# Performance work log

Hardware: AMD Instinct MI355X
Metric: run time of the kernel (lower is better)

The kernel has to match this reference:

```python
import jax, jax.numpy as jnp
import numpy as np
from jax import lax

B, C, W = 16, 64, 125000  # batch, EEG channels, raw samples
KH, KW, SW, OC = 3, 2500, 1250, 32


def setup_inputs() -> dict:
    key = jax.random.key(0)
    ks = jax.random.split(key, 10)
    inp = {
        "x": jax.random.normal(ks[0], (B, 1, C, W), dtype=jnp.float32),
        # Conv2d(1->32, kernel=(3,2500))
        "conv_w": jax.random.normal(ks[1], (OC, 1, KH, KW), dtype=jnp.float32) * 0.02,
        "conv_b": jax.random.normal(ks[2], (OC,), dtype=jnp.float32) * 0.02,
        # Conv2d(32->1, kernel=(1,1))
        "conv2_w": jax.random.normal(ks[3], (1, OC, 1, 1), dtype=jnp.float32) * 0.1,
        "conv2_b": jax.random.normal(ks[4], (1,), dtype=jnp.float32) * 0.1,
        # nn.RNN(input_size=1, hidden_size=1): scalar weights
        "w_ih": jax.random.normal(ks[5], (1, 1), dtype=jnp.float32),
        "w_hh": jax.random.normal(ks[6], (1, 1), dtype=jnp.float32),
        "b_ih": jax.random.normal(ks[7], (1,), dtype=jnp.float32) * 0.1,
        "b_hh": jax.random.normal(ks[8], (1,), dtype=jnp.float32) * 0.1,
        # torch.rand(num_layers=1, B, 1) hidden init, reused for every row i
        "h0": jax.random.uniform(ks[9], (1, B, 1), dtype=jnp.float32),
    }
    return inp


def reference(x, conv_w, conv_b, conv2_w, conv2_b, w_ih, w_hh, b_ih, b_hh, h0):
    # F.pad(x, (0,0,1,1), 'replicate'): pad channel (height) dim by 1 each side
    xp = jnp.pad(x, ((0, 0), (0, 0), (1, 1), (0, 0)), mode="edge")
    # conv + relu -> [B, 32, C, T]
    y = lax.conv_general_dilated(
        xp, conv_w, window_strides=(1, SW), padding="VALID",
        dimension_numbers=("NCHW", "OIHW", "NCHW"))
    y = jax.nn.relu(y + conv_b[None, :, None, None])
    # 1x1 conv 32->1 + relu -> [B, C, T]
    z = jnp.einsum("bohw,o->bhw", y, conv2_w[0, :, 0, 0]) + conv2_b[0]
    z = jax.nn.relu(z)
    # Elman RNN with scalar weights, scanned over T; carry is [B, C]
    wih, whh = w_ih[0, 0], w_hh[0, 0]
    bias = b_ih[0] + b_hh[0]
    h_init = jnp.broadcast_to(h0[0, :, 0][:, None], z.shape[:2])  # [B, C]

    def step(h, xt):  # xt: [B, C]
        h = jnp.tanh(wih * xt + whh * h + bias)
        return h, None

    xs = jnp.moveaxis(z, -1, 0)  # [T, B, C]
    h_final, _ = lax.scan(step, h_init, xs)
    return jax.nn.sigmoid(h_final)  # [B, C]
```

## Files before the change

kernel.cpp:

```cpp
#include <hip/hip_runtime.h>
#include <math.h>

#define B_ 16
#define C_ 64
#define J_ 100
#define T_ 99
#define KW_ 1250
#define KP_ 1280
#define N_ 192
#define M_ (B_*C_*J_)
#define BM 128
#define BK 32
#define NCHUNK 40

typedef __attribute__((ext_vector_type(8))) _Float16 half8;
typedef __attribute__((ext_vector_type(4))) float f32x4;
typedef __attribute__((ext_vector_type(2), aligned(8))) float f32x2;

#define GLD_LDS16(gp, lp) \
    __builtin_amdgcn_global_load_lds((const __attribute__((address_space(1))) void*)(gp), \
                                     (__attribute__((address_space(3))) void*)(lp), 16, 0, 0)

__global__ __launch_bounds__(256) void wconv_kernel(const float* __restrict__ cw,
                                                    _Float16* __restrict__ wh)
{
    int n = blockIdx.x;
    int o = n / 6, rem = n - o * 6, kh = rem >> 1, hf = rem & 1;
    const float* src = cw + o * 7500 + kh * 2500 + hf * 1250;
    for (int k = threadIdx.x; k < KP_; k += 256)
        wh[n * KP_ + k] = (k < KW_) ? (_Float16)src[k] : (_Float16)0.f;
}

__global__ __launch_bounds__(256, 2) void gemm_kernel(const float* __restrict__ x,
                                                      const _Float16* __restrict__ wh,
                                                      _Float16* __restrict__ P)
{
    __shared__ __align__(16) _Float16 smA[2][BM * BK];
    __shared__ __align__(16) _Float16 smB[3][N_ * BK];

    const int tid  = threadIdx.x;
    const int bm0  = blockIdx.x * BM;
    const int lane = tid & 63;
    const int wave = tid >> 6;
    const int wm   = (wave & 1) * 64;
    const int wn   = (wave >> 1) * 96;
    const int l15  = lane & 15;
    const int lq   = lane >> 4;

    const float* ap[2]; int koff[2]; int adst[2];
#pragma unroll
    for (int u = 0; u < 2; u++) {
        int q  = u * 256 + tid;
        int rl = q >> 2, p = q & 3;
        int gr = bm0 + rl;
        int b  = gr / 6400;
        int j  = (gr - b * 6400) >> 6;
        int c  = gr & 63;
        long xrow = (long)(b * 64 + c) * 100 + j;
        ap[u]   = x + xrow * KW_ + p * 8;
        koff[u] = p * 8;
        adst[u] = q * 8;
    }
    const _Float16* bp[3]; int bdst[3];
#pragma unroll
    for (int i = 0; i < 3; i++) {
        int qb = (i * 4 + wave) * 64 + lane;
        int n = qb >> 2, p = qb & 3;
        bp[i]   = wh + n * KP_ + p * 8;
        bdst[i] = (i * 4 + wave) * 512;
    }

    f32x4 acc[4][6];
#pragma unroll
    for (int mi = 0; mi < 4; mi++)
#pragma unroll
        for (int ni = 0; ni < 6; ni++) acc[mi][ni] = (f32x4){0.f, 0.f, 0.f, 0.f};

    f32x2 areg[2][2][4];
#define LOADA(k0, slot)                                                        \
    do {                                                                       \
        _Pragma("unroll") for (int u = 0; u < 2; u++)                          \
        _Pragma("unroll") for (int j2 = 0; j2 < 4; j2++) {                     \
            int k = (k0) + koff[u] + j2 * 2;           \
            areg[slot][u][j2] = (k + 2 <= KW_)                                 \
                ? *(const f32x2*)(ap[u] + (k0) + j2 * 2)                       \
                : (f32x2){0.f, 0.f};                                           \
        }                                                                      \
    } while (0)

#pragma unroll
    for (int i = 0; i < 3; i++) GLD_LDS16(bp[i], &smB[0][0] + bdst[i]);
#pragma unroll
    for (int i = 0; i < 3; i++) GLD_LDS16(bp[i] + BK, &smB[1][0] + bdst[i]);
    LOADA(0, 0);
    LOADA(BK, 1);

    int bi = 0;
    for (int ck = 0; ck < NCHUNK; ck++) {
        const int slot = ck & 1;
        _Float16* Ab = &smA[slot][0];
        _Float16* Bb = &smB[bi][0];

#pragma unroll
        for (int u = 0; u < 2; u++) {
            half8 h;
#pragma unroll
            for (int j2 = 0; j2 < 4; j2++) {
                h[2 * j2]     = (_Float16)areg[slot][u][j2].x;
                h[2 * j2 + 1] = (_Float16)areg[slot][u][j2].y;
            }
            *(half8*)(Ab + adst[u]) = h;
        }

        asm volatile("s_waitcnt lgkmcnt(0)" ::: "memory");
        if (ck == 0 || ck >= NCHUNK - 2) {
            asm volatile("s_waitcnt vmcnt(0)" ::: "memory");
        } else {
            asm volatile("s_waitcnt vmcnt(11)" ::: "memory");
        }
        __builtin_amdgcn_s_barrier();
        __builtin_amdgcn_sched_barrier(0);

        int bi2 = bi + 2; if (bi2 >= 3) bi2 -= 3;
        if (ck + 2 < NCHUNK) {
            _Float16* Bn = &smB[bi2][0];
            const int k2 = (ck + 2) * BK;
#pragma unroll
            for (int i = 0; i < 3; i++) GLD_LDS16(bp[i] + k2, Bn + bdst[i]);
        }
        if (ck + 2 < NCHUNK) LOADA((ck + 2) * BK, slot);

        half8 afr[4], bfr[6];
#pragma unroll
        for (int mi = 0; mi < 4; mi++)
            afr[mi] = *(const half8*)(Ab + (wm + mi * 16 + l15) * BK + lq * 8);
#pragma unroll
        for (int ni = 0; ni < 6; ni++)
            bfr[ni] = *(const half8*)(Bb + (wn + ni * 16 + l15) * BK + lq * 8);
#pragma unroll
        for (int mi = 0; mi < 4; mi++)
#pragma unroll
            for (int ni = 0; ni < 6; ni++)
                acc[mi][ni] = __builtin_amdgcn_mfma_f32_16x16x32_f16(
                    afr[mi], bfr[ni], acc[mi][ni], 0, 0, 0);

        bi = (bi == 2) ? 0 : bi + 1;
    }

#pragma unroll
    for (int mi = 0; mi < 4; mi++) {
        int mrow = bm0 + wm + mi * 16 + lq * 4;
#pragma unroll
        for (int ni = 0; ni < 6; ni++) {
            int n = wn + ni * 16 + l15;
#pragma unroll
            for (int r2 = 0; r2 < 4; r2++)
                P[(size_t)(mrow + r2) * N_ + n] = (_Float16)acc[mi][ni][r2];
        }
    }
#undef LOADA
}

__global__ __launch_bounds__(256) void combine_kernel(const _Float16* __restrict__ P,
                                                      const float* __restrict__ conv_b,
                                                      const float* __restrict__ c2w,
                                                      const float* __restrict__ c2b,
                                                      float* __restrict__ z)
{
    __shared__ float Pl[64][193];
    __shared__ float red[4][64];
    const int t   = blockIdx.x;
    const int b   = blockIdx.y;
    const int tid = threadIdx.x;
    const int c   = tid & 63;
    const int og  = tid >> 6;

    float v[8];
#pragma unroll
    for (int o = 0; o < 8; o++) v[o] = conv_b[og * 8 + o];

    for (int hf = 0; hf < 2; hf++) {
        const int j = t + hf;
        const _Float16* Pb = P + (size_t)((b * 100 + j) * 64) * N_;
        __syncthreads();
#pragma unroll
        for (int i = 0; i < 6; i++) {
            int e   = i * 256 + tid;
            half8 h = *(const half8*)(Pb + e * 8);
            int row = e / 24;
            int col = (e - row * 24) * 8;
#pragma unroll
            for (int u = 0; u < 8; u++) Pl[row][col + u] = (float)h[u];
        }
        __syncthreads();
#pragma unroll
        for (int kh = 0; kh < 3; kh++) {
            int r = c + kh - 1;
            r = r < 0 ? 0 : (r > 63 ? 63 : r);
#pragma unroll
            for (int o = 0; o < 8; o++)
                v[o] += Pl[r][(og * 8 + o) * 6 + kh * 2 + hf];
        }
    }

    float part = 0.f;
#pragma unroll
    for (int o = 0; o < 8; o++) part += fmaxf(v[o], 0.f) * c2w[og * 8 + o];
    red[og][c] = part;
    __syncthreads();
    if (og == 0) {
        float zz = red[0][c] + red[1][c] + red[2][c] + red[3][c] + c2b[0];
        z[t * (B_ * C_) + b * 64 + c] = fmaxf(zz, 0.f);
    }
}

__global__ __launch_bounds__(256) void rnn_kernel(const float* __restrict__ z,
                                                  const float* __restrict__ w_ih,
                                                  const float* __restrict__ w_hh,
                                                  const float* __restrict__ b_ih,
                                                  const float* __restrict__ b_hh,
                                                  const float* __restrict__ h0,
                                                  float* __restrict__ out)
{
    int g = blockIdx.x * 256 + threadIdx.x;
    if (g >= B_ * C_) return;
    int b = g >> 6;
    const float wih  = w_ih[0];
    const float whh  = w_hh[0];
    const float bias = b_ih[0] + b_hh[0];
    float h = h0[b];
    for (int t = 0; t < T_; t++)
        h = tanhf(fmaf(wih, z[t * (B_ * C_) + g], fmaf(whh, h, bias)));
    out[g] = 1.f / (1.f + expf(-h));
}

extern "C" void kernel_launch(void* const* d_in, const int* in_sizes, int n_in,
                              void* d_out, int out_size, void* d_ws, size_t ws_size,
                              hipStream_t stream)
{
    const float* x   = (const float*)d_in[0];
    const float* cw  = (const float*)d_in[1];
    const float* cb  = (const float*)d_in[2];
    const float* c2w = (const float*)d_in[3];
    const float* c2b = (const float*)d_in[4];
    const float* wih = (const float*)d_in[5];
    const float* whh = (const float*)d_in[6];
    const float* bih = (const float*)d_in[7];
    const float* bhh = (const float*)d_in[8];
    const float* h0  = (const float*)d_in[9];
    float* out = (float*)d_out;

    const size_t whbytes = (size_t)N_ * KP_ * sizeof(_Float16);
    const size_t pbytes  = (size_t)M_ * N_ * sizeof(_Float16);
    const size_t zbytes  = (size_t)B_ * C_ * T_ * sizeof(float);

    if (ws_size < whbytes + pbytes + zbytes) return;

    _Float16* wh = (_Float16*)d_ws;
    _Float16* P  = (_Float16*)((char*)d_ws + whbytes);
    float*    z  = (float*)((char*)d_ws + whbytes + pbytes);

    wconv_kernel<<<N_, 256, 0, stream>>>(cw, wh);
    gemm_kernel<<<M_ / BM, 256, 0, stream>>>(x, wh, P);
    combine_kernel<<<dim3(T_, B_), 256, 0, stream>>>(P, cb, c2w, c2b, z);
    rnn_kernel<<<4, 256, 0, stream>>>(z, wih, whh, bih, bhh, h0, out);
}
```

Before: 808.9 us.

## Load GEMM B fragments directly from global memory and stage RNN inputs in LDS

The GEMM drops the triple-buffered LDS staging of the fp16 weight tile. Each wave now reads its B fragments straight from global memory (L2-resident) with a one-ahead register prefetch, and the A prefetch depth drops from two chunks to one. The LDS saving is used to raise launch bounds to 3 blocks per CU for higher occupancy. The RNN kernel batches its z loads into shared memory in chunks of 50 timesteps, so the serial tanh chain no longer stalls on a global load every step. The risks are more global or L2 traffic for B, because each wave rereads weights, and less latency hiding from the shallower prefetch.

Result: slower. 860.0 us (+6.3%).

```diff
diff --git a/kernel.cpp b/kernel.cpp
--- a/kernel.cpp
+++ b/kernel.cpp
@@ -17,10 +17,6 @@
 typedef __attribute__((ext_vector_type(4))) float f32x4;
 typedef __attribute__((ext_vector_type(2), aligned(8))) float f32x2;
 
-#define GLD_LDS16(gp, lp) \
-    __builtin_amdgcn_global_load_lds((const __attribute__((address_space(1))) void*)(gp), \
-                                     (__attribute__((address_space(3))) void*)(lp), 16, 0, 0)
-
 __global__ __launch_bounds__(256) void wconv_kernel(const float* __restrict__ cw,
                                                     _Float16* __restrict__ wh)
 {
@@ -31,12 +27,11 @@
         wh[n * KP_ + k] = (k < KW_) ? (_Float16)src[k] : (_Float16)0.f;
 }
 
-__global__ __launch_bounds__(256, 2) void gemm_kernel(const float* __restrict__ x,
+__global__ __launch_bounds__(256, 3) void gemm_kernel(const float* __restrict__ x,
                                                       const _Float16* __restrict__ wh,
                                                       _Float16* __restrict__ P)
 {
     __shared__ __align__(16) _Float16 smA[2][BM * BK];
-    __shared__ __align__(16) _Float16 smB[3][N_ * BK];
 
     const int tid  = threadIdx.x;
     const int bm0  = blockIdx.x * BM;
@@ -61,14 +56,7 @@
         koff[u] = p * 8;
         adst[u] = q * 8;
     }
-    const _Float16* bp[3]; int bdst[3];
-#pragma unroll
-    for (int i = 0; i < 3; i++) {
-        int qb = (i * 4 + wave) * 64 + lane;
-        int n = qb >> 2, p = qb & 3;
-        bp[i]   = wh + n * KP_ + p * 8;
-        bdst[i] = (i * 4 + wave) * 512;
-    }
+    const _Float16* bbase = wh + (size_t)(wn + l15) * KP_ + lq * 8;
 
     f32x4 acc[4][6];
 #pragma unroll
@@ -76,75 +64,60 @@
 #pragma unroll
         for (int ni = 0; ni < 6; ni++) acc[mi][ni] = (f32x4){0.f, 0.f, 0.f, 0.f};
 
-    f32x2 areg[2][2][4];
-#define LOADA(k0, slot)                                                        \
+    f32x2 areg[2][4];
+#define LOADA(k0)                                                              \
     do {                                                                       \
         _Pragma("unroll") for (int u = 0; u < 2; u++)                          \
         _Pragma("unroll") for (int j2 = 0; j2 < 4; j2++) {                     \
             int k = (k0) + koff[u] + j2 * 2;           \
-            areg[slot][u][j2] = (k + 2 <= KW_)                                 \
+            areg[u][j2] = (k + 2 <= KW_)                                       \
                 ? *(const f32x2*)(ap[u] + (k0) + j2 * 2)                       \
                 : (f32x2){0.f, 0.f};                                           \
         }                                                                      \
     } while (0)
 
-#pragma unroll
-    for (int i = 0; i < 3; i++) GLD_LDS16(bp[i], &smB[0][0] + bdst[i]);
-#pragma unroll
-    for (int i = 0; i < 3; i++) GLD_LDS16(bp[i] + BK, &smB[1][0] + bdst[i]);
-    LOADA(0, 0);
-    LOADA(BK, 1);
-
-    int bi = 0;
+    LOADA(0);
+
     for (int ck = 0; ck < NCHUNK; ck++) {
         const int slot = ck & 1;
         _Float16* Ab = &smA[slot][0];
-        _Float16* Bb = &smB[bi][0];
+
+        half8 bcur = *(const half8*)(bbase + (size_t)ck * BK);
 
 #pragma unroll
         for (int u = 0; u < 2; u++) {
             half8 h;
 #pragma unroll
             for (int j2 = 0; j2 < 4; j2++) {
-                h[2 * j2]     = (_Float16)areg[slot][u][j2].x;
-                h[2 * j2 + 1] = (_Float16)areg[slot][u][j2].y;
+                h[2 * j2]     = (_Float16)areg[u][j2].x;
+                h[2 * j2 + 1] = (_Float16)areg[u][j2].y;
             }
             *(half8*)(Ab + adst[u]) = h;
         }
 
         asm volatile("s_waitcnt lgkmcnt(0)" ::: "memory");
-        if (ck == 0 || ck >= NCHUNK - 2) {
-            asm volatile("s_waitcnt vmcnt(0)" ::: "memory");
-        } else {
-            asm volatile("s_waitcnt vmcnt(11)" ::: "memory");
-        }
         __builtin_amdgcn_s_barrier();
         __builtin_amdgcn_sched_barrier(0);
 
-        int bi2 = bi + 2; if (bi2 >= 3) bi2 -= 3;
-        if (ck + 2 < NCHUNK) {
-            _Float16* Bn = &smB[bi2][0];
-            const int k2 = (ck + 2) * BK;
-#pragma unroll
-            for (int i = 0; i < 3; i++) GLD_LDS16(bp[i] + k2, Bn + bdst[i]);
-        }
-        if (ck + 2 < NCHUNK) LOADA((ck + 2) * BK, slot);
-
-        half8 afr[4], bfr[6];
+        if (ck + 1 < NCHUNK) LOADA((ck + 1) * BK);
+
+        half8 afr[4];
 #pragma unroll
         for (int mi = 0; mi < 4; mi++)
             afr[mi] = *(const half8*)(Ab + (wm + mi * 16 + l15) * BK + lq * 8);
-#pragma unroll
-        for (int ni = 0; ni < 6; ni++)
-            bfr[ni] = *(const half8*)(Bb + (wn + ni * 16 + l15) * BK + lq * 8);
-#pragma unroll
-        for (int mi = 0; mi < 4; mi++)
-#pragma unroll
-            for (int ni = 0; ni < 6; ni++)
+
+#pragma unroll
+        for (int ni = 0; ni < 6; ni++) {
+            half8 bnext = bcur;
+            if (ni < 5)
+                bnext = *(const half8*)(bbase + (size_t)(ni + 1) * 16 * KP_
+                                              + (size_t)ck * BK);
+#pragma unroll
+            for (int mi = 0; mi < 4; mi++)
                 acc[mi][ni] = __builtin_amdgcn_mfma_f32_16x16x32_f16(
-                    afr[mi], bfr[ni], acc[mi][ni], 0, 0, 0);
-
-        bi = (bi == 2) ? 0 : bi + 1;
+                    afr[mi], bcur, acc[mi][ni], 0, 0, 0);
+            bcur = bnext;
+        }
     }
 
 #pragma unroll
@@ -222,15 +195,23 @@
                                                   const float* __restrict__ h0,
                                                   float* __restrict__ out)
 {
-    int g = blockIdx.x * 256 + threadIdx.x;
-    if (g >= B_ * C_) return;
-    int b = g >> 6;
+    __shared__ float zs[50][256];
+    const int tid = threadIdx.x;
+    const int g   = blockIdx.x * 256 + tid;
+    const int b   = g >> 6;
     const float wih  = w_ih[0];
     const float whh  = w_hh[0];
     const float bias = b_ih[0] + b_hh[0];
     float h = h0[b];
-    for (int t = 0; t < T_; t++)
-        h = tanhf(fmaf(wih, z[t * (B_ * C_) + g], fmaf(whh, h, bias)));
+    for (int t0 = 0; t0 < T_; t0 += 50) {
+        const int nt = (T_ - t0) < 50 ? (T_ - t0) : 50;
+        __syncthreads();
+        for (int tt = 0; tt < nt; tt++)
+            zs[tt][tid] = z[(t0 + tt) * (B_ * C_) + g];
+        __syncthreads();
+        for (int tt = 0; tt < nt; tt++)
+            h = tanhf(fmaf(wih, zs[tt][tid], fmaf(whh, h, bias)));
+    }
     out[g] = 1.f / (1.f + expf(-h));
 }
 
```
